# Optimization experiments

Hardware: AMD Instinct MI355X
Metric: run time of the kernel (lower is better)

Reference implementation:

```python
import jax, jax.numpy as jnp
import numpy as np

B, L_IN, D = 4, 4096, 1024
R_MIN, R_MAX = 0.9, 0.999


def setup_inputs() -> dict:
    key = jax.random.key(0)
    k0, k1, k2 = jax.random.split(key, 3)
    inputs = jax.random.normal(k0, (B, L_IN, D), jnp.float32)
    Wi = jax.random.normal(k1, (2 * D, D), jnp.float32) / np.sqrt(D)
    bi = jnp.zeros((2 * D,), jnp.float32)
    Wo = jax.random.normal(k2, (D, 2 * D), jnp.float32) / np.sqrt(2 * D)
    bo = jnp.zeros((D,), jnp.float32)
    # LRU stable-ring initialization, exactly as in the torch module
    rng = np.random.default_rng(0)
    u1 = rng.random(D)
    u2 = rng.random(D)
    v_log = np.log(-0.5 * np.log(u1 * (R_MAX ** 2 - R_MIN ** 2) + R_MIN ** 2))
    theta_log = np.log(u2 * np.pi * 2)
    gamma_log = np.log(np.sqrt(1.0 - np.exp(-np.exp(v_log)) ** 2))
    params_log = jnp.asarray(np.stack([v_log, theta_log, gamma_log]), jnp.float32)
    return {"inputs": inputs, "Wi": Wi, "bi": bi, "Wo": Wo, "bo": bo,
            "params_log": params_log}


def _lru_forward(inputs, Wi, bi, Wo, bo, params_log):
    b, l_in, d = inputs.shape
    u = inputs @ Wi.T + bi                      # [B, L, 2D]
    v, theta, gamma = jnp.exp(params_log)       # each [D]
    # torch.view_as_complex: interleaved (real, imag) pairs along last dim
    uc = u.reshape(b, l_in, d, 2)
    x = jax.lax.complex(uc[..., 0], uc[..., 1])  # [B, L, D] complex64
    log2_L = int(np.ceil(np.log2(l_in)))
    L = 2 ** log2_L
    x = jnp.pad(x, ((0, 0), (0, L - l_in), (0, 0)))
    # Blelloch-style log-depth scan: x_t = lambda * x_{t-1} + u_t,
    # lambda = exp(-v + i*theta)
    for i in range(1, log2_L + 1):
        blk = 2 ** i
        xb = x.reshape(b * L // blk, blk, d)
        x1, x2 = xb[:, : blk // 2], xb[:, blk // 2:]
        pos = jnp.arange(1, blk // 2 + 1, dtype=jnp.float32)  # [blk/2]
        lambs = jnp.exp(jax.lax.complex(-pos[:, None] * v,
                                        pos[:, None] * theta))  # [blk/2, D]
        x2 = x2 + lambs * x1[:, -1:]
        x = jnp.concatenate([x1, x2], axis=1).reshape(b, L, d)
    x = x[:, :l_in] * gamma.astype(x.dtype)     # normalize, drop padding
    xr = jnp.concatenate([x.real, x.imag], axis=-1)  # [B, L, 2D]
    out = xr @ Wo.T + bo
    return jax.nn.relu(out)


def reference(inputs, Wi, bi, Wo, bo, params_log):
    return _lru_forward(inputs, Wi, bi, Wo, bo, params_log)
```

## Files before the change

kernel.cpp:

```cpp
#include <hip/hip_runtime.h>

#define BB 4
#define LL 4096
#define DD 1024
#define SS 64
#define TT 64

typedef __attribute__((ext_vector_type(4))) float  floatx4;
typedef __attribute__((ext_vector_type(8))) short  shortx8;

static __device__ __forceinline__ unsigned short f2bf(float f) {
    unsigned int u = __float_as_uint(f);
    u += 0x7fffu + ((u >> 16) & 1u);
    return (unsigned short)(u >> 16);
}
static __device__ __forceinline__ float bf2f(unsigned short h) {
    return __uint_as_float(((unsigned int)h) << 16);
}

#define NIN4 (BB * LL * DD / 4)
#define NW4  (2 * DD * DD / 4)
__global__ void cast_all_kernel(const float4* __restrict__ s_in, ushort4* __restrict__ d_inb,
                                const float4* __restrict__ s_wi, ushort4* __restrict__ d_wib,
                                const float4* __restrict__ s_wo, ushort4* __restrict__ d_wob) {
    int i = blockIdx.x * blockDim.x + threadIdx.x;
    const float4* s; ushort4* d; int j;
    if (i < NIN4)                 { s = s_in; d = d_inb; j = i; }
    else if (i < NIN4 + NW4)      { s = s_wi; d = d_wib; j = i - NIN4; }
    else                          { s = s_wo; d = d_wob; j = i - NIN4 - NW4; }
    float4 v = s[j];
    ushort4 o;
    o.x = f2bf(v.x); o.y = f2bf(v.y); o.z = f2bf(v.z); o.w = f2bf(v.w);
    d[j] = o;
}

template<int K, int NT, int EPI>
__global__ __launch_bounds__(512, 2)
void gemm256(const unsigned short* __restrict__ A,
             const unsigned short* __restrict__ B,
             const float* __restrict__ bias,
             void* __restrict__ Cp) {
    constexpr int N   = NT * 256;
    constexpr int NKT = K / 64;
    __shared__ __align__(16) short As[2][256 * 64];
    __shared__ __align__(16) short Bs[2][256 * 64];

    const int tid = threadIdx.x;
    const int blk = blockIdx.x;
    const int xcd = blk & 7;
    const int i2  = blk >> 3;
    const int tileM = ((i2 / NT) * 8 + xcd) * 256;
    const int tileN = (i2 % NT) * 256;

    const int lane   = tid & 63;
    const int wave   = tid >> 6;
    const int wave_m = wave >> 2;
    const int wave_n = wave & 3;
    const int r16    = lane & 15;
    const int quad   = lane >> 4;
    const int slotx  = r16 & 7;
    const int wmRow  = wave_m * 64 + r16;
    const int wnRow  = wave_n * 32 + r16;

    const int srow = tid >> 3;
    const int scol = ((tid & 7) ^ (srow & 7)) * 8;
    const int ldsChunkBase = (tid & ~63) * 8;
    const size_t aOff = (size_t)(tileM + srow) * K + scol;
    const size_t bOff = (size_t)(tileN + srow) * K + scol;

    floatx4 acc[8][4] = {};
    shortx8 af[4][2], bf0v[2][2], bf1v[2][2];

#define GLL(SRC, DST) __builtin_amdgcn_global_load_lds( \
        (const __attribute__((address_space(1))) void*)(SRC), \
        (__attribute__((address_space(3))) void*)(DST), 16, 0, 0)
#define STAGE_A(BUF, H, KT) do { \
    GLL(A + aOff + (size_t)((H) * 128) * K + (KT) * 64,      &As[BUF][(H) * 8192 + ldsChunkBase]); \
    GLL(A + aOff + (size_t)((H) * 128 + 64) * K + (KT) * 64, &As[BUF][(H) * 8192 + 4096 + ldsChunkBase]); \
} while (0)
#define STAGE_B(BUF, H, KT) do { \
    GLL(B + bOff + (size_t)((H) * 128) * K + (KT) * 64,      &Bs[BUF][(H) * 8192 + ldsChunkBase]); \
    GLL(B + bOff + (size_t)((H) * 128 + 64) * K + (KT) * 64, &Bs[BUF][(H) * 8192 + 4096 + ldsChunkBase]); \
} while (0)
#define LOAD_A(BUF, MH) do { \
    _Pragma("unroll") for (int il = 0; il < 4; ++il) \
    _Pragma("unroll") for (int kk = 0; kk < 2; ++kk) \
        af[il][kk] = *(const shortx8*)&As[BUF][((MH) * 128 + wmRow + il * 16) * 64 + ((kk * 4 + quad) ^ slotx) * 8]; \
} while (0)
#define LOAD_B(BUF, NH, DST) do { \
    _Pragma("unroll") for (int jl = 0; jl < 2; ++jl) \
    _Pragma("unroll") for (int kk = 0; kk < 2; ++kk) \
        DST[jl][kk] = *(const shortx8*)&Bs[BUF][((NH) * 128 + wnRow + jl * 16) * 64 + ((kk * 4 + quad) ^ slotx) * 8]; \
} while (0)
#define MFMAQ(MH, NH, BF) do { \
    __builtin_amdgcn_s_setprio(1); \
    _Pragma("unroll") for (int kk = 0; kk < 2; ++kk) \
    _Pragma("unroll") for (int il = 0; il < 4; ++il) \
    _Pragma("unroll") for (int jl = 0; jl < 2; ++jl) \
        acc[(MH) * 4 + il][(NH) * 2 + jl] = __builtin_amdgcn_mfma_f32_16x16x32_bf16( \
            af[il][kk], BF[jl][kk], acc[(MH) * 4 + il][(NH) * 2 + jl], 0, 0, 0); \
    __builtin_amdgcn_s_setprio(0); \
} while (0)
#define BAR()  __builtin_amdgcn_s_barrier()
#define LGKM0() asm volatile("s_waitcnt lgkmcnt(0)" ::: "memory")

    STAGE_A(0, 0, 0);
    STAGE_B(0, 0, 0);
    STAGE_B(0, 1, 0);
    STAGE_A(0, 1, 0);
    STAGE_A(1, 0, 1);
    STAGE_B(1, 1, 1);
    STAGE_A(1, 1, 1);
    asm volatile("s_waitcnt vmcnt(6)" ::: "memory");
    BAR();
    LOAD_A(0, 0);
    LOAD_B(0, 0, bf0v);

#pragma unroll 2
    for (int t = 0; t < NKT; ++t) {
        const int cb = t & 1;
        const int t1 = (t + 1 < NKT) ? t + 1 : NKT - 1;
        const int t2 = (t + 2 < NKT) ? t + 2 : NKT - 1;
        BAR();
        LGKM0();
        STAGE_B(cb ^ 1, 0, t1);
        MFMAQ(0, 0, bf0v);
        LOAD_B(cb, 1, bf1v);
        BAR();
        LGKM0();
        STAGE_A(cb, 0, t2);
        MFMAQ(0, 1, bf1v);
        LOAD_A(cb, 1);
        BAR();
        LGKM0();
        STAGE_B(cb, 1, t2);
        MFMAQ(1, 0, bf0v);
        asm volatile("s_waitcnt vmcnt(4)" ::: "memory");
        BAR();
        STAGE_A(cb, 1, t2);
        MFMAQ(1, 1, bf1v);
        LOAD_A(cb ^ 1, 0);
        LOAD_B(cb ^ 1, 0, bf0v);
    }
    asm volatile("s_waitcnt vmcnt(0) lgkmcnt(0)" ::: "memory");

#pragma unroll
    for (int i = 0; i < 8; ++i) {
        const int row0 = tileM + (i >> 2) * 128 + wave_m * 64 + (i & 3) * 16 + quad * 4;
#pragma unroll
        for (int j = 0; j < 4; ++j) {
            const int col = tileN + (j >> 1) * 128 + wave_n * 32 + (j & 1) * 16 + r16;
            const float bv = bias[col];
#pragma unroll
            for (int r = 0; r < 4; ++r) {
                float v = acc[i][j][r] + bv;
                if (EPI == 0) {
                    ((unsigned short*)Cp)[(size_t)(row0 + r) * N + col] = f2bf(v);
                } else {
                    ((float*)Cp)[(size_t)(row0 + r) * N + col] = fmaxf(v, 0.0f);
                }
            }
        }
    }
#undef GLL
#undef STAGE_A
#undef STAGE_B
#undef LOAD_A
#undef LOAD_B
#undef MFMAQ
#undef BAR
#undef LGKM0
}

__global__ __launch_bounds__(256)
void scanA(const unsigned short* __restrict__ u,
           const float* __restrict__ plog,
           float2* __restrict__ Eend) {
    const int d0 = (blockIdx.x * 256 + threadIdx.x) * 2;
    const int c = blockIdx.y, b = blockIdx.z;
    const float v0  = expf(plog[d0]),      v1  = expf(plog[d0 + 1]);
    const float th0 = expf(plog[DD + d0]), th1 = expf(plog[DD + d0 + 1]);
    const float a0 = expf(-v0), a1 = expf(-v1);
    const float lr0 = a0 * cosf(th0), li0 = a0 * sinf(th0);
    const float lr1 = a1 * cosf(th1), li1 = a1 * sinf(th1);
    float zr0 = 0.f, zi0 = 0.f, zr1 = 0.f, zi1 = 0.f;
    const unsigned short* up = u + (size_t)(b * LL + c * TT) * (2 * DD) + 2 * d0;
#pragma unroll 4
    for (int tl = 0; tl < TT; ++tl) {
        uint2 pr = *(const uint2*)up;
        float xr0 = bf2f((unsigned short)(pr.x & 0xffffu));
        float xi0 = bf2f((unsigned short)(pr.x >> 16));
        float xr1 = bf2f((unsigned short)(pr.y & 0xffffu));
        float xi1 = bf2f((unsigned short)(pr.y >> 16));
        float t;
        t = lr0 * zr0 - li0 * zi0 + xr0; zi0 = lr0 * zi0 + li0 * zr0 + xi0; zr0 = t;
        t = lr1 * zr1 - li1 * zi1 + xr1; zi1 = lr1 * zi1 + li1 * zr1 + xi1; zr1 = t;
        up += 2 * DD;
    }
    *(float4*)&Eend[(size_t)c * (BB * DD) + b * DD + d0] =
        make_float4(zr0, zi0, zr1, zi1);
}

__global__ __launch_bounds__(256)
void scanC(const unsigned short* __restrict__ u,
           const float* __restrict__ plog,
           const float2* __restrict__ Eend,
           unsigned short* __restrict__ xr) {
    const int d0 = (blockIdx.x * 256 + threadIdx.x) * 2;
    const int c = blockIdx.y, b = blockIdx.z;
    const float v0  = expf(plog[d0]),      v1  = expf(plog[d0 + 1]);
    const float th0 = expf(plog[DD + d0]), th1 = expf(plog[DD + d0 + 1]);
    const float g0  = expf(plog[2 * DD + d0]), g1 = expf(plog[2 * DD + d0 + 1]);
    const float a0 = expf(-v0), a1 = expf(-v1);
    const float lr0 = a0 * cosf(th0), li0 = a0 * sinf(th0);
    const float lr1 = a1 * cosf(th1), li1 = a1 * sinf(th1);

    const float aT0 = expf(-(float)TT * v0), aT1 = expf(-(float)TT * v1);
    const float Lr0 = aT0 * cosf((float)TT * th0), Li0 = aT0 * sinf((float)TT * th0);
    const float Lr1 = aT1 * cosf((float)TT * th1), Li1 = aT1 * sinf((float)TT * th1);
    float yr0 = 0.f, yi0 = 0.f, yr1 = 0.f, yi1 = 0.f;
    for (int cc = 0; cc < c; ++cc) {
        float4 e = *(const float4*)&Eend[(size_t)cc * (BB * DD) + b * DD + d0];
        float t;
        t = Lr0 * yr0 - Li0 * yi0 + e.x; yi0 = Lr0 * yi0 + Li0 * yr0 + e.y; yr0 = t;
        t = Lr1 * yr1 - Li1 * yi1 + e.z; yi1 = Lr1 * yi1 + Li1 * yr1 + e.w; yr1 = t;
    }

    const unsigned short* up = u + (size_t)(b * LL + c * TT) * (2 * DD) + 2 * d0;
    unsigned short* xp = xr + (size_t)(b * LL + c * TT) * (2 * DD) + d0;
#pragma unroll 4
    for (int tl = 0; tl < TT; ++tl) {
        uint2 pr = *(const uint2*)up;
        float xr0 = bf2f((unsigned short)(pr.x & 0xffffu));
        float xi0 = bf2f((unsigned short)(pr.x >> 16));
        float xr1 = bf2f((unsigned short)(pr.y & 0xffffu));
        float xi1 = bf2f((unsigned short)(pr.y >> 16));
        float t;
        t = lr0 * yr0 - li0 * yi0 + xr0; yi0 = lr0 * yi0 + li0 * yr0 + xi0; yr0 = t;
        t = lr1 * yr1 - li1 * yi1 + xr1; yi1 = lr1 * yi1 + li1 * yr1 + xi1; yr1 = t;
        *(unsigned int*)&xp[0]  = (unsigned int)f2bf(g0 * yr0) |
                                  ((unsigned int)f2bf(g1 * yr1) << 16);
        *(unsigned int*)&xp[DD] = (unsigned int)f2bf(g0 * yi0) |
                                  ((unsigned int)f2bf(g1 * yi1) << 16);
        up += 2 * DD;
        xp += 2 * DD;
    }
}

extern "C" void kernel_launch(void* const* d_in, const int* in_sizes, int n_in,
                              void* d_out, int out_size, void* d_ws, size_t ws_size,
                              hipStream_t stream) {
    const float* inputs = (const float*)d_in[0];
    const float* Wi     = (const float*)d_in[1];
    const float* bi     = (const float*)d_in[2];
    const float* Wo     = (const float*)d_in[3];
    const float* bo     = (const float*)d_in[4];
    const float* plog   = (const float*)d_in[5];
    float* out = (float*)d_out;

    const size_t M = (size_t)BB * LL;
    unsigned short* u_bf  = (unsigned short*)d_ws;
    unsigned short* xr_bf = u_bf  + M * 2 * DD;
    unsigned short* in_bf = xr_bf + M * 2 * DD;
    unsigned short* Wi_bf = in_bf + M * DD;
    unsigned short* Wo_bf = Wi_bf + (size_t)2 * DD * DD;
    float2* Eend = (float2*)(Wo_bf + (size_t)2 * DD * DD);

    {
        int total4 = NIN4 + 2 * NW4;
        cast_all_kernel<<<total4 / 256, 256, 0, stream>>>(
            (const float4*)inputs, (ushort4*)in_bf,
            (const float4*)Wi,     (ushort4*)Wi_bf,
            (const float4*)Wo,     (ushort4*)Wo_bf);
    }

    gemm256<DD, 8, 0><<<(M / 256) * 8, 512, 0, stream>>>(
        in_bf, Wi_bf, bi, (void*)u_bf);

    scanA<<<dim3(DD / 512, SS, BB), 256, 0, stream>>>(u_bf, plog, Eend);
    scanC<<<dim3(DD / 512, SS, BB), 256, 0, stream>>>(u_bf, plog, Eend, xr_bf);

    gemm256<2 * DD, 4, 1><<<(M / 256) * 4, 512, 0, stream>>>(
        xr_bf, Wo_bf, bo, (void*)out);
}
```

Baseline: 305.1 us.

## Interleave LDS reads with MFMAs via sched_group_barrier and double-buffer B fragments

Replaces the unroll-2 GEMM main loop with an explicit two-tile macro body. It adds sched_group_barrier patterns so the compiler interleaves LDS fragment reads between MFMA instructions. The B fragments are double-buffered so the next tile's B0 load can be issued during the third quarter rather than at the end. The vmcnt wait is also relaxed from 4 to 2 outstanding loads. The intent is to hide LDS latency behind matrix math, at the cost of higher register pressure and tighter reliance on the wait counts being correct.

```diff
diff --git a/kernel.cpp b/kernel.cpp
--- a/kernel.cpp
+++ b/kernel.cpp
@@ -69,40 +69,79 @@
     const size_t bOff = (size_t)(tileN + srow) * K + scol;
 
     floatx4 acc[8][4] = {};
-    shortx8 af[4][2], bf0v[2][2], bf1v[2][2];
+    shortx8 af[4][2], b0f[2][2][2], b1f[2][2];
 
 #define GLL(SRC, DST) __builtin_amdgcn_global_load_lds( \
         (const __attribute__((address_space(1))) void*)(SRC), \
         (__attribute__((address_space(3))) void*)(DST), 16, 0, 0)
 #define STAGE_A(BUF, H, KT) do { \
-    GLL(A + aOff + (size_t)((H) * 128) * K + (KT) * 64,      &As[BUF][(H) * 8192 + ldsChunkBase]); \
-    GLL(A + aOff + (size_t)((H) * 128 + 64) * K + (KT) * 64, &As[BUF][(H) * 8192 + 4096 + ldsChunkBase]); \
+    GLL(A + aOff + (size_t)((H) * 128) * K + (KT) * 64,      &As[(BUF)][(H) * 8192 + ldsChunkBase]); \
+    GLL(A + aOff + (size_t)((H) * 128 + 64) * K + (KT) * 64, &As[(BUF)][(H) * 8192 + 4096 + ldsChunkBase]); \
 } while (0)
 #define STAGE_B(BUF, H, KT) do { \
-    GLL(B + bOff + (size_t)((H) * 128) * K + (KT) * 64,      &Bs[BUF][(H) * 8192 + ldsChunkBase]); \
-    GLL(B + bOff + (size_t)((H) * 128 + 64) * K + (KT) * 64, &Bs[BUF][(H) * 8192 + 4096 + ldsChunkBase]); \
+    GLL(B + bOff + (size_t)((H) * 128) * K + (KT) * 64,      &Bs[(BUF)][(H) * 8192 + ldsChunkBase]); \
+    GLL(B + bOff + (size_t)((H) * 128 + 64) * K + (KT) * 64, &Bs[(BUF)][(H) * 8192 + 4096 + ldsChunkBase]); \
 } while (0)
 #define LOAD_A(BUF, MH) do { \
+    _Pragma("unroll") for (int kk = 0; kk < 2; ++kk) \
     _Pragma("unroll") for (int il = 0; il < 4; ++il) \
+        af[il][kk] = *(const shortx8*)&As[(BUF)][((MH) * 128 + wmRow + il * 16) * 64 + ((kk * 4 + quad) ^ slotx) * 8]; \
+} while (0)
+#define LOAD_B(BUF, NH, DST) do { \
     _Pragma("unroll") for (int kk = 0; kk < 2; ++kk) \
-        af[il][kk] = *(const shortx8*)&As[BUF][((MH) * 128 + wmRow + il * 16) * 64 + ((kk * 4 + quad) ^ slotx) * 8]; \
-} while (0)
-#define LOAD_B(BUF, NH, DST) do { \
     _Pragma("unroll") for (int jl = 0; jl < 2; ++jl) \
-    _Pragma("unroll") for (int kk = 0; kk < 2; ++kk) \
-        DST[jl][kk] = *(const shortx8*)&Bs[BUF][((NH) * 128 + wnRow + jl * 16) * 64 + ((kk * 4 + quad) ^ slotx) * 8]; \
+        DST[jl][kk] = *(const shortx8*)&Bs[(BUF)][((NH) * 128 + wnRow + jl * 16) * 64 + ((kk * 4 + quad) ^ slotx) * 8]; \
 } while (0)
 #define MFMAQ(MH, NH, BF) do { \
-    __builtin_amdgcn_s_setprio(1); \
     _Pragma("unroll") for (int kk = 0; kk < 2; ++kk) \
     _Pragma("unroll") for (int il = 0; il < 4; ++il) \
     _Pragma("unroll") for (int jl = 0; jl < 2; ++jl) \
         acc[(MH) * 4 + il][(NH) * 2 + jl] = __builtin_amdgcn_mfma_f32_16x16x32_bf16( \
             af[il][kk], BF[jl][kk], acc[(MH) * 4 + il][(NH) * 2 + jl], 0, 0, 0); \
+} while (0)
+#define BAR()   __builtin_amdgcn_s_barrier()
+#define LGKM0() asm volatile("s_waitcnt lgkmcnt(0)" ::: "memory")
+#define SGB(M, NN) __builtin_amdgcn_sched_group_barrier(M, NN, 0)
+#define S41() do { SGB(0x8, 4); SGB(0x100, 1); } while (0)
+#define S21() do { SGB(0x8, 2); SGB(0x100, 1); } while (0)
+#define PAT41() do { S41(); S41(); S41(); S41(); } while (0)
+#define PAT21() do { S21(); S21(); S21(); S21(); S21(); S21(); S21(); S21(); } while (0)
+
+#define TILE(P, T1, T2) do { \
+     \
+    BAR(); LGKM0(); \
+    STAGE_B((P) ^ 1, 0, (T1)); \
+    __builtin_amdgcn_s_setprio(1); \
+    MFMAQ(0, 0, b0f[(P)]); \
+    LOAD_B((P), 1, b1f); \
+    PAT41(); \
     __builtin_amdgcn_s_setprio(0); \
-} while (0)
-#define BAR()  __builtin_amdgcn_s_barrier()
-#define LGKM0() asm volatile("s_waitcnt lgkmcnt(0)" ::: "memory")
+     \
+    BAR(); LGKM0(); \
+    STAGE_A((P), 0, (T2)); \
+    __builtin_amdgcn_s_setprio(1); \
+    MFMAQ(0, 1, b1f); \
+    LOAD_A((P), 1); \
+    PAT21(); \
+    __builtin_amdgcn_s_setprio(0); \
+     \
+    asm volatile("s_waitcnt vmcnt(2)" ::: "memory"); \
+    BAR(); LGKM0(); \
+    STAGE_B((P), 1, (T2)); \
+    __builtin_amdgcn_s_setprio(1); \
+    MFMAQ(1, 0, b0f[(P)]); \
+    LOAD_B((P) ^ 1, 0, b0f[(P) ^ 1]); \
+    PAT41(); \
+    __builtin_amdgcn_s_setprio(0); \
+     \
+    BAR(); \
+    STAGE_A((P), 1, (T2)); \
+    __builtin_amdgcn_s_setprio(1); \
+    MFMAQ(1, 1, b1f); \
+    LOAD_A((P) ^ 1, 0); \
+    PAT21(); \
+    __builtin_amdgcn_s_setprio(0); \
+} while (0)
 
     STAGE_A(0, 0, 0);
     STAGE_B(0, 0, 0);
@@ -114,33 +153,15 @@
     asm volatile("s_waitcnt vmcnt(6)" ::: "memory");
     BAR();
     LOAD_A(0, 0);
-    LOAD_B(0, 0, bf0v);
-
-#pragma unroll 2
-    for (int t = 0; t < NKT; ++t) {
-        const int cb = t & 1;
-        const int t1 = (t + 1 < NKT) ? t + 1 : NKT - 1;
-        const int t2 = (t + 2 < NKT) ? t + 2 : NKT - 1;
-        BAR();
-        LGKM0();
-        STAGE_B(cb ^ 1, 0, t1);
-        MFMAQ(0, 0, bf0v);
-        LOAD_B(cb, 1, bf1v);
-        BAR();
-        LGKM0();
-        STAGE_A(cb, 0, t2);
-        MFMAQ(0, 1, bf1v);
-        LOAD_A(cb, 1);
-        BAR();
-        LGKM0();
-        STAGE_B(cb, 1, t2);
-        MFMAQ(1, 0, bf0v);
-        asm volatile("s_waitcnt vmcnt(4)" ::: "memory");
-        BAR();
-        STAGE_A(cb, 1, t2);
-        MFMAQ(1, 1, bf1v);
-        LOAD_A(cb ^ 1, 0);
-        LOAD_B(cb ^ 1, 0, bf0v);
+    LOAD_B(0, 0, b0f[0]);
+
+    for (int t = 0; t < NKT; t += 2) {
+        const int e1 = (t + 1 < NKT) ? t + 1 : NKT - 1;
+        const int e2 = (t + 2 < NKT) ? t + 2 : NKT - 1;
+        TILE(0, e1, e2);
+        const int o1 = (t + 2 < NKT) ? t + 2 : NKT - 1;
+        const int o2 = (t + 3 < NKT) ? t + 3 : NKT - 1;
+        TILE(1, o1, o2);
     }
     asm volatile("s_waitcnt vmcnt(0) lgkmcnt(0)" ::: "memory");
 
@@ -170,6 +191,12 @@
 #undef MFMAQ
 #undef BAR
 #undef LGKM0
+#undef SGB
+#undef S41
+#undef S21
+#undef PAT41
+#undef PAT21
+#undef TILE
 }
 
 __global__ __launch_bounds__(256)
```

New measurement: 313.8 us. 1.03x slower.

## Restructure chunked scan into three phases with a separate carry-propagation kernel

Applied to the files above, without the earlier changes.

Adds a scanB kernel that computes each chunk's exclusive carry in a single sequential pass, replacing the O(c) carry recomputation inside every scanC block. Chunks shrink from 64 to 32 timesteps (128 chunks), and each thread handles one channel instead of two, giving 4x more threads in the scan kernels. Eend now reuses the in_bf workspace, which is dead after the first GEMM. The costs are an extra launch, narrower per-thread loads and stores (2-byte writes), and a serial 128-step loop in scanB.

```diff
diff --git a/kernel.cpp b/kernel.cpp
--- a/kernel.cpp
+++ b/kernel.cpp
@@ -3,8 +3,8 @@
 #define BB 4
 #define LL 4096
 #define DD 1024
-#define SS 64
-#define TT 64
+#define SS 128
+#define TT 32
 
 typedef __attribute__((ext_vector_type(4))) float  floatx4;
 typedef __attribute__((ext_vector_type(8))) short  shortx8;
@@ -176,72 +176,74 @@
 void scanA(const unsigned short* __restrict__ u,
            const float* __restrict__ plog,
            float2* __restrict__ Eend) {
-    const int d0 = (blockIdx.x * 256 + threadIdx.x) * 2;
+    const int d = blockIdx.x * 256 + threadIdx.x;
     const int c = blockIdx.y, b = blockIdx.z;
-    const float v0  = expf(plog[d0]),      v1  = expf(plog[d0 + 1]);
-    const float th0 = expf(plog[DD + d0]), th1 = expf(plog[DD + d0 + 1]);
-    const float a0 = expf(-v0), a1 = expf(-v1);
-    const float lr0 = a0 * cosf(th0), li0 = a0 * sinf(th0);
-    const float lr1 = a1 * cosf(th1), li1 = a1 * sinf(th1);
-    float zr0 = 0.f, zi0 = 0.f, zr1 = 0.f, zi1 = 0.f;
-    const unsigned short* up = u + (size_t)(b * LL + c * TT) * (2 * DD) + 2 * d0;
-#pragma unroll 4
+    const float v  = expf(plog[d]);
+    const float th = expf(plog[DD + d]);
+    const float a  = expf(-v);
+    const float lr = a * cosf(th), li = a * sinf(th);
+    float zr = 0.f, zi = 0.f;
+    const unsigned short* up = u + (size_t)(b * LL + c * TT) * (2 * DD) + 2 * d;
+#pragma unroll 8
     for (int tl = 0; tl < TT; ++tl) {
-        uint2 pr = *(const uint2*)up;
-        float xr0 = bf2f((unsigned short)(pr.x & 0xffffu));
-        float xi0 = bf2f((unsigned short)(pr.x >> 16));
-        float xr1 = bf2f((unsigned short)(pr.y & 0xffffu));
-        float xi1 = bf2f((unsigned short)(pr.y >> 16));
-        float t;
-        t = lr0 * zr0 - li0 * zi0 + xr0; zi0 = lr0 * zi0 + li0 * zr0 + xi0; zr0 = t;
-        t = lr1 * zr1 - li1 * zi1 + xr1; zi1 = lr1 * zi1 + li1 * zr1 + xi1; zr1 = t;
+        unsigned int pr = *(const unsigned int*)up;
+        float xr = bf2f((unsigned short)(pr & 0xffffu));
+        float xi = bf2f((unsigned short)(pr >> 16));
+        float t = lr * zr - li * zi + xr;
+        zi = lr * zi + li * zr + xi;
+        zr = t;
         up += 2 * DD;
     }
-    *(float4*)&Eend[(size_t)c * (BB * DD) + b * DD + d0] =
-        make_float4(zr0, zi0, zr1, zi1);
+    Eend[(size_t)c * (BB * DD) + b * DD + d] = make_float2(zr, zi);
+}
+
+__global__ __launch_bounds__(256)
+void scanB(const float* __restrict__ plog, float2* __restrict__ E) {
+    const int i = blockIdx.x * 256 + threadIdx.x;
+    const int d = i & (DD - 1);
+    const float v  = expf(plog[d]);
+    const float th = expf(plog[DD + d]);
+    const float aT = expf(-(float)TT * v);
+    const float Lr = aT * cosf((float)TT * th), Li = aT * sinf((float)TT * th);
+    float yr = 0.f, yi = 0.f;
+    float2* p = E + i;
+#pragma unroll 8
+    for (int c = 0; c < SS; ++c) {
+        float2 e = *p;
+        *p = make_float2(yr, yi);
+        float t = Lr * yr - Li * yi + e.x;
+        yi = Lr * yi + Li * yr + e.y;
+        yr = t;
+        p += BB * DD;
+    }
 }
 
 __global__ __launch_bounds__(256)
 void scanC(const unsigned short* __restrict__ u,
            const float* __restrict__ plog,
-           const float2* __restrict__ Eend,
+           const float2* __restrict__ Carry,
            unsigned short* __restrict__ xr) {
-    const int d0 = (blockIdx.x * 256 + threadIdx.x) * 2;
+    const int d = blockIdx.x * 256 + threadIdx.x;
     const int c = blockIdx.y, b = blockIdx.z;
-    const float v0  = expf(plog[d0]),      v1  = expf(plog[d0 + 1]);
-    const float th0 = expf(plog[DD + d0]), th1 = expf(plog[DD + d0 + 1]);
-    const float g0  = expf(plog[2 * DD + d0]), g1 = expf(plog[2 * DD + d0 + 1]);
-    const float a0 = expf(-v0), a1 = expf(-v1);
-    const float lr0 = a0 * cosf(th0), li0 = a0 * sinf(th0);
-    const float lr1 = a1 * cosf(th1), li1 = a1 * sinf(th1);
-
-    const float aT0 = expf(-(float)TT * v0), aT1 = expf(-(float)TT * v1);
-    const float Lr0 = aT0 * cosf((float)TT * th0), Li0 = aT0 * sinf((float)TT * th0);
-    const float Lr1 = aT1 * cosf((float)TT * th1), Li1 = aT1 * sinf((float)TT * th1);
-    float yr0 = 0.f, yi0 = 0.f, yr1 = 0.f, yi1 = 0.f;
-    for (int cc = 0; cc < c; ++cc) {
-        float4 e = *(const float4*)&Eend[(size_t)cc * (BB * DD) + b * DD + d0];
-        float t;
-        t = Lr0 * yr0 - Li0 * yi0 + e.x; yi0 = Lr0 * yi0 + Li0 * yr0 + e.y; yr0 = t;
-        t = Lr1 * yr1 - Li1 * yi1 + e.z; yi1 = Lr1 * yi1 + Li1 * yr1 + e.w; yr1 = t;
-    }
-
-    const unsigned short* up = u + (size_t)(b * LL + c * TT) * (2 * DD) + 2 * d0;
-    unsigned short* xp = xr + (size_t)(b * LL + c * TT) * (2 * DD) + d0;
-#pragma unroll 4
+    const float v  = expf(plog[d]);
+    const float th = expf(plog[DD + d]);
+    const float g  = expf(plog[2 * DD + d]);
+    const float a  = expf(-v);
+    const float lr = a * cosf(th), li = a * sinf(th);
+    const float2 cy = Carry[(size_t)c * (BB * DD) + b * DD + d];
+    float yr = cy.x, yi = cy.y;
+    const unsigned short* up = u + (size_t)(b * LL + c * TT) * (2 * DD) + 2 * d;
+    unsigned short* xp = xr + (size_t)(b * LL + c * TT) * (2 * DD) + d;
+#pragma unroll 8
     for (int tl = 0; tl < TT; ++tl) {
-        uint2 pr = *(const uint2*)up;
-        float xr0 = bf2f((unsigned short)(pr.x & 0xffffu));
-        float xi0 = bf2f((unsigned short)(pr.x >> 16));
-        float xr1 = bf2f((unsigned short)(pr.y & 0xffffu));
-        float xi1 = bf2f((unsigned short)(pr.y >> 16));
-        float t;
-        t = lr0 * yr0 - li0 * yi0 + xr0; yi0 = lr0 * yi0 + li0 * yr0 + xi0; yr0 = t;
-        t = lr1 * yr1 - li1 * yi1 + xr1; yi1 = lr1 * yi1 + li1 * yr1 + xi1; yr1 = t;
-        *(unsigned int*)&xp[0]  = (unsigned int)f2bf(g0 * yr0) |
-                                  ((unsigned int)f2bf(g1 * yr1) << 16);
-        *(unsigned int*)&xp[DD] = (unsigned int)f2bf(g0 * yi0) |
-                                  ((unsigned int)f2bf(g1 * yi1) << 16);
+        unsigned int pr = *(const unsigned int*)up;
+        float xrv = bf2f((unsigned short)(pr & 0xffffu));
+        float xiv = bf2f((unsigned short)(pr >> 16));
+        float t = lr * yr - li * yi + xrv;
+        yi = lr * yi + li * yr + xiv;
+        yr = t;
+        xp[0]  = f2bf(g * yr);
+        xp[DD] = f2bf(g * yi);
         up += 2 * DD;
         xp += 2 * DD;
     }
@@ -264,7 +266,7 @@
     unsigned short* in_bf = xr_bf + M * 2 * DD;
     unsigned short* Wi_bf = in_bf + M * DD;
     unsigned short* Wo_bf = Wi_bf + (size_t)2 * DD * DD;
-    float2* Eend = (float2*)(Wo_bf + (size_t)2 * DD * DD);
+    float2* Eend = (float2*)in_bf;
 
     {
         int total4 = NIN4 + 2 * NW4;
@@ -277,8 +279,9 @@
     gemm256<DD, 8, 0><<<(M / 256) * 8, 512, 0, stream>>>(
         in_bf, Wi_bf, bi, (void*)u_bf);
 
-    scanA<<<dim3(DD / 512, SS, BB), 256, 0, stream>>>(u_bf, plog, Eend);
-    scanC<<<dim3(DD / 512, SS, BB), 256, 0, stream>>>(u_bf, plog, Eend, xr_bf);
+    scanA<<<dim3(DD / 256, SS, BB), 256, 0, stream>>>(u_bf, plog, Eend);
+    scanB<<<(BB * DD) / 256, 256, 0, stream>>>(plog, Eend);
+    scanC<<<dim3(DD / 256, SS, BB), 256, 0, stream>>>(u_bf, plog, Eend, xr_bf);
 
     gemm256<2 * DD, 4, 1><<<(M / 256) * 4, 512, 0, stream>>>(
         xr_bf, Wo_bf, bo, (void*)out);
```

New measurement: 294.9 us. 1.03x faster.
